# Kernel tuning notes

Hardware: AMD Instinct MI355X
Metric: run time of the kernel (lower is better)

Reference implementation:

```python
import jax, jax.numpy as jnp
import numpy as np

N = 50000          # nodes per side (variables == clauses here)
IN, HID, OUT = 64, 128, 128
H = 4              # attention heads (self and cross)
P = 2              # num_meta_paths
E = 640000         # edges per graph
NEG = 0.2          # leaky_relu negative slope


def _glorot(key, shape):
    fan = shape[-2] + shape[-1]
    return (jax.random.normal(key, shape) * jnp.sqrt(2.0 / fan)).astype(jnp.float32)


def _ln(x, g, b):
    mu = x.mean(-1, keepdims=True)
    v = ((x - mu) ** 2).mean(-1, keepdims=True)
    return (x - mu) / jnp.sqrt(v + 1e-5) * g + b


def _segment_softmax(s, seg, num):
    # s: [E, H]; softmax over edges sharing the same seg id
    smax = jax.ops.segment_max(s, seg, num_segments=num)
    e = jnp.exp(s - smax[seg])
    den = jax.ops.segment_sum(e, seg, num_segments=num)
    return e / (den[seg] + 1e-16)


def _agg(alpha, feats, src, dst, num):
    # out[d, h, c] = sum_{e: dst[e]=d} alpha[e,h] * feats[src[e], c]
    gathered = feats[src]  # [E, C]
    outs = [jax.ops.segment_sum(alpha[:, h:h + 1] * gathered, dst, num_segments=num)
            for h in range(alpha.shape[1])]
    return jnp.stack(outs, axis=1)  # [num, H, C]


def _hga_self(x, adj, W, att_l, att_r, bias):
    # homogeneous HGAConv with self loops, concat=False (mean over heads)
    n = x.shape[0]
    xl = x @ W.T                      # [N, C]
    al = xl @ att_l                   # [N, H]
    ar = xl @ att_r                   # [N, H]
    loops = jnp.arange(n)
    src = jnp.concatenate([adj[0], loops])
    dst = jnp.concatenate([adj[1], loops])
    score = al[dst] + ar[src]         # edge_score: a_l[adj[1]] + a_r[adj[0]]
    alpha = _segment_softmax(jax.nn.leaky_relu(score, NEG), dst, n)
    out = _agg(alpha, xl, src, dst, n).mean(axis=1)  # [N, C]
    return out + bias


def _hga_cross(xv, xc, adj, Wl, Wr, att_l, att_r, bias):
    # bipartite HGAConv: adj[1] indexes var nodes, adj[0] indexes cls nodes
    n, m = xv.shape[0], xc.shape[0]
    xl = xv @ Wl.T
    xr = xc @ Wr.T
    al = xl @ att_l
    ar = xr @ att_r
    ar_ = xl @ att_r
    al_ = xr @ att_l
    c_idx, v_idx = adj[0], adj[1]
    score = al[v_idx] + ar[c_idx]        # -> normalized per var node
    score_ = ar_[v_idx] + al_[c_idx]     # transposed direction -> per cls node
    alpha = _segment_softmax(jax.nn.leaky_relu(score, NEG), v_idx, n)
    alpha_ = _segment_softmax(jax.nn.leaky_relu(score_, NEG), c_idx, m)
    out_var = _agg(alpha, xr, c_idx, v_idx, n).mean(axis=1) + bias   # [n, OUT]
    out_cls = _agg(alpha_, xl, v_idx, c_idx, m).mean(axis=1) + bias  # [m, OUT]
    return out_var, out_cls


def setup_inputs() -> dict:
    key = jax.random.key(0)
    ks = jax.random.split(key, 32)
    d = {}
    d['x_var'] = jax.random.normal(ks[0], (N, IN), dtype=jnp.float32)
    d['x_cls'] = jax.random.normal(ks[1], (N, IN), dtype=jnp.float32)
    d['mp_var'] = jax.random.randint(ks[2], (P, 2, E), 0, N)
    d['mp_cls'] = jax.random.randint(ks[3], (P, 2, E), 0, N)
    d['adj_pos'] = jax.random.randint(ks[4], (2, E), 0, N)
    d['adj_neg'] = jax.random.randint(ks[5], (2, E), 0, N)
    d['W_var_emb'] = _glorot(ks[6], (HID, IN))
    d['W_cls_emb'] = _glorot(ks[7], (HID, IN))
    d['ln_var_g'] = jnp.ones(HID); d['ln_var_b'] = jnp.zeros(HID)
    d['ln_cls_g'] = jnp.ones(HID); d['ln_cls_b'] = jnp.zeros(HID)
    d['var_pw'] = jnp.ones(P); d['cls_pw'] = jnp.ones(P)
    d['sv_W'] = _glorot(ks[8], (P, HID, HID))
    d['sv_al'] = _glorot(ks[9], (P, HID, H))
    d['sv_ar'] = _glorot(ks[10], (P, HID, H))
    d['sv_b'] = jnp.zeros((P, HID))
    d['sc_W'] = _glorot(ks[11], (P, HID, HID))
    d['sc_al'] = _glorot(ks[12], (P, HID, H))
    d['sc_ar'] = _glorot(ks[13], (P, HID, H))
    d['sc_b'] = jnp.zeros((P, HID))
    d['cp_Wl'] = _glorot(ks[14], (OUT, HID))
    d['cp_Wr'] = _glorot(ks[15], (OUT, HID))
    d['cp_al'] = _glorot(ks[16], (OUT, H))
    d['cp_ar'] = _glorot(ks[17], (OUT, H))
    d['cp_b'] = jnp.zeros(OUT)
    d['cn_Wl'] = _glorot(ks[18], (OUT, HID))
    d['cn_Wr'] = _glorot(ks[19], (OUT, HID))
    d['cn_al'] = _glorot(ks[20], (OUT, H))
    d['cn_ar'] = _glorot(ks[21], (OUT, H))
    d['cn_b'] = jnp.zeros(OUT)
    return d


def reference(x_var, x_cls, mp_var, mp_cls, adj_pos, adj_neg,
              W_var_emb, W_cls_emb, ln_var_g, ln_var_b, ln_cls_g, ln_cls_b,
              var_pw, cls_pw, sv_W, sv_al, sv_ar, sv_b, sc_W, sc_al, sc_ar, sc_b,
              cp_Wl, cp_Wr, cp_al, cp_ar, cp_b, cn_Wl, cn_Wr, cn_al, cn_ar, cn_b):
    xv = x_var @ W_var_emb.T          # [N, HID]
    xc = x_cls @ W_cls_emb.T
    # pre-norm residual self-attention, weighted sum over meta paths
    hv = _ln(xv, ln_var_g, ln_var_b)
    hc = _ln(xc, ln_cls_g, ln_cls_b)
    av = sum(var_pw[p] * _hga_self(hv, mp_var[p], sv_W[p], sv_al[p], sv_ar[p], sv_b[p]) for p in range(P))
    ac = sum(cls_pw[p] * _hga_self(hc, mp_cls[p], sc_W[p], sc_al[p], sc_ar[p], sc_b[p]) for p in range(P))
    xv = xv + av
    xc = xc + ac
    # bipartite cross attention over positive / negative literal edges
    vpos, cpos = _hga_cross(xv, xc, adj_pos, cp_Wl, cp_Wr, cp_al, cp_ar, cp_b)
    vneg, cneg = _hga_cross(xv, xc, adj_neg, cn_Wl, cn_Wr, cn_al, cn_ar, cn_b)
    return jnp.stack([vpos + vneg, cpos + cneg])  # [2, N, OUT]
```

## Files before the change

kernel.cpp:

```cpp
#include <hip/hip_runtime.h>
#include <hip/hip_bf16.h>

#define NN 50000
#define EE 640000
#define NEG 0.2f
#define CAP 128

#define BSH 9
#define NBKT 98
#define FCAP 7168
#define CHUNKA 8192
#define PA_B 79

struct Ptr8 { const int* p[8]; };
struct MArgs { const float* w[8]; const float* al[8]; const float* ar[8]; };

struct SegArg {
    const int* starts;
    const int* counts;
    const unsigned short* srt;
    const float* adst;
    const float* asrc;
    const unsigned short* feats;
    const float* pw;
    int pwi;
    int hasLoop;
};

typedef __attribute__((ext_vector_type(8))) short short8;
typedef __attribute__((ext_vector_type(8))) unsigned short ushort8;
typedef __attribute__((ext_vector_type(4))) float floatx4;

__device__ __forceinline__ unsigned short f2bf(float x) {
    unsigned b = __float_as_uint(x);
    b = b + 0x7fffu + ((b >> 16) & 1u);
    return (unsigned short)(b >> 16);
}

__global__ void transpose_emb(const float* __restrict__ wev, const float* __restrict__ wec,
                              float* __restrict__ out)
{
    int i = blockIdx.x * 256 + threadIdx.x;
    if (i < 8192) { out[i] = wev[(i & 127) * 64 + (i >> 7)]; return; }
    if (i < 16384) { int j = i - 8192; out[i] = wec[(j & 127) * 64 + (j >> 7)]; }
}

__global__ void make_M(MArgs a, float* __restrict__ Mbuf)
{
    int b = blockIdx.x;
    const float* W  = a.w[b];
    const float* AL = a.al[b];
    const float* AR = a.ar[b];
    for (int e = threadIdx.x; e < 1024; e += 256) {
        int k = e >> 3, h = e & 7;
        const float* att = (h < 4) ? AL : AR;
        int hh = h & 3;
        float s = 0.f;
        for (int c = 0; c < 128; c++) s += W[c * 128 + k] * att[c * 4 + hh];
        Mbuf[b * 1024 + e] = s;
    }
}

__global__ void embed_ln(const float* __restrict__ x, const float* __restrict__ Wt,
                         const float* __restrict__ g, const float* __restrict__ b,
                         const float* __restrict__ pw, const float* __restrict__ sb,
                         float* __restrict__ F, float* __restrict__ C)
{
    __shared__ float lx[8][64];
    __shared__ float red[2][8][2];
    int c = threadIdx.x;
    int n0 = blockIdx.x * 8;
    for (int t = c; t < 8 * 64; t += 128) {
        lx[t >> 6][t & 63] = x[(size_t)(n0 + (t >> 6)) * 64 + (t & 63)];
    }
    __syncthreads();
    float acc[8];
#pragma unroll
    for (int m = 0; m < 8; m++) acc[m] = 0.f;
    for (int k = 0; k < 64; k++) {
        float w = Wt[k * 128 + c];
#pragma unroll
        for (int m = 0; m < 8; m++) acc[m] += lx[m][k] * w;
    }
    int lane = c & 63, wv = c >> 6;
#pragma unroll
    for (int m = 0; m < 8; m++) {
        float s1 = acc[m], s2 = acc[m] * acc[m];
        for (int off = 32; off; off >>= 1) { s1 += __shfl_xor(s1, off); s2 += __shfl_xor(s2, off); }
        if (lane == 0) { red[wv][m][0] = s1; red[wv][m][1] = s2; }
    }
    __syncthreads();
    float biassum = pw[0] * sb[c] + pw[1] * sb[128 + c];
    float gg = g[c], bb = b[c];
#pragma unroll
    for (int m = 0; m < 8; m++) {
        float s1 = red[0][m][0] + red[1][m][0];
        float s2 = red[0][m][1] + red[1][m][1];
        float mu  = s1 * (1.f / 128.f);
        float var = s2 * (1.f / 128.f) - mu * mu;
        float inv = rsqrtf(var + 1e-5f);
        float v = acc[m];
        size_t idx = (size_t)(n0 + m) * 128 + c;
        F[idx] = v + biassum;
        C[idx] = (v - mu) * inv * gg + bb;
    }
}

__device__ __forceinline__ void stage_W(const float* __restrict__ W,
                                        unsigned short* __restrict__ WL, int t)
{
    for (int i = t; i < 2048; i += 256) {
        int n = i >> 4, c16 = i & 15;
        const float* src = W + n * 128 + c16 * 8;
        short8 v;
#pragma unroll
        for (int j = 0; j < 8; j++) v[j] = (short)f2bf(src[j]);
        *(short8*)&WL[(n * 16 + (c16 ^ (n & 15))) * 8] = v;
    }
}

__global__ __launch_bounds__(256) void mfma_proj2(
    const float* __restrict__ in,
    const float* __restrict__ W0, const float* __restrict__ W1,
    const float* __restrict__ M0, const float* __restrict__ M1,
    unsigned short* __restrict__ ob0, unsigned short* __restrict__ ob1,
    float4* __restrict__ dl0, float4* __restrict__ dr0,
    float4* __restrict__ dl1, float4* __restrict__ dr1)
{
    __shared__ unsigned short WL[16384];
    __shared__ float ML[2048];

    int t = threadIdx.x;
    stage_W(W0, WL, t);
    for (int i = t; i < 1024; i += 256) { ML[i] = M0[i]; ML[1024 + i] = M1[i]; }
    __syncthreads();

    int w = t >> 6, lane = t & 63;
    int ln = lane & 15, quad = lane >> 4;
    int rbase = blockIdx.x * 64 + w * 16;
    int row = rbase + ln;
    int arow = (row < NN) ? row : (NN - 1);

    short8 afrag[4];
    float p[16];
#pragma unroll
    for (int h = 0; h < 16; h++) p[h] = 0.f;
#pragma unroll
    for (int kc = 0; kc < 4; kc++) {
        int k0 = kc * 32 + quad * 8;
        const float* ap = in + (size_t)arow * 128 + k0;
        float av[8];
#pragma unroll
        for (int j = 0; j < 8; j++) av[j] = ap[j];
#pragma unroll
        for (int j = 0; j < 8; j++) {
            afrag[kc][j] = (short)f2bf(av[j]);
            const float* m0 = &ML[(k0 + j) * 8];
            const float* m1 = &ML[1024 + (k0 + j) * 8];
#pragma unroll
            for (int h = 0; h < 8; h++) { p[h] += av[j] * m0[h]; p[8 + h] += av[j] * m1[h]; }
        }
    }
#pragma unroll
    for (int h = 0; h < 16; h++) {
        p[h] += __shfl_xor(p[h], 16);
        p[h] += __shfl_xor(p[h], 32);
    }
    if (quad == 0 && row < NN) {
        dl0[row] = make_float4(p[0], p[1], p[2], p[3]);
        dr0[row] = make_float4(p[4], p[5], p[6], p[7]);
        dl1[row] = make_float4(p[8], p[9], p[10], p[11]);
        dr1[row] = make_float4(p[12], p[13], p[14], p[15]);
    }

#pragma unroll
    for (int ct = 0; ct < 8; ct++) {
        floatx4 acc = {0.f, 0.f, 0.f, 0.f};
#pragma unroll
        for (int kc = 0; kc < 4; kc++) {
            int c16 = kc * 4 + quad;
            int n = ct * 16 + ln;
            short8 bfr = *(const short8*)&WL[(n * 16 + (c16 ^ ln)) * 8];
            acc = __builtin_amdgcn_mfma_f32_16x16x32_bf16(afrag[kc], bfr, acc, 0, 0, 0);
        }
#pragma unroll
        for (int r = 0; r < 4; r++) {
            int rr = rbase + quad * 4 + r;
            if (rr < NN) ob0[(size_t)rr * 128 + ct * 16 + ln] = f2bf(acc[r]);
        }
    }
    __syncthreads();
    stage_W(W1, WL, t);
    __syncthreads();
#pragma unroll
    for (int ct = 0; ct < 8; ct++) {
        floatx4 acc = {0.f, 0.f, 0.f, 0.f};
#pragma unroll
        for (int kc = 0; kc < 4; kc++) {
            int c16 = kc * 4 + quad;
            int n = ct * 16 + ln;
            short8 bfr = *(const short8*)&WL[(n * 16 + (c16 ^ ln)) * 8];
            acc = __builtin_amdgcn_mfma_f32_16x16x32_bf16(afrag[kc], bfr, acc, 0, 0, 0);
        }
#pragma unroll
        for (int r = 0; r < 4; r++) {
            int rr = rbase + quad * 4 + r;
            if (rr < NN) ob1[(size_t)rr * 128 + ct * 16 + ln] = f2bf(acc[r]);
        }
    }
}

__global__ void zero_bcnt(int* __restrict__ p)
{
    int i = blockIdx.x * 256 + threadIdx.x;
    if (i < 8 * NBKT) p[i] = 0;
}

__global__ void bucket_count(Ptr8 dst, int* __restrict__ bcnt)
{
    __shared__ int h[NBKT];
    int l = blockIdx.x / PA_B, cb = blockIdx.x % PA_B;
    const int* dp = dst.p[l];
    for (int i = threadIdx.x; i < NBKT; i += 256) h[i] = 0;
    __syncthreads();
    int e0 = cb * CHUNKA;
    for (int i = threadIdx.x; i < CHUNKA; i += 256) {
        int e = e0 + i;
        if (e < EE) atomicAdd(&h[dp[e] >> BSH], 1);
    }
    __syncthreads();
    for (int i = threadIdx.x; i < NBKT; i += 256)
        if (h[i]) atomicAdd(&bcnt[l * NBKT + i], h[i]);
}

__global__ void bucket_scan(const int* __restrict__ bcnt, int* __restrict__ bstart,
                            int* __restrict__ bcur)
{
    __shared__ int sh[NBKT];
    int l = blockIdx.x;
    for (int i = threadIdx.x; i < NBKT; i += 256) sh[i] = bcnt[l * NBKT + i];
    __syncthreads();
    if (threadIdx.x == 0) {
        int acc = 0;
        for (int i = 0; i < NBKT; i++) { int t = sh[i]; sh[i] = acc; acc += t; }
    }
    __syncthreads();
    for (int i = threadIdx.x; i < NBKT; i += 256) {
        bstart[l * (NBKT + 1) + i] = sh[i];
        bcur[l * NBKT + i] = sh[i];
    }
    if (threadIdx.x == 0) bstart[l * (NBKT + 1) + NBKT] = EE;
}

__global__ void bucket_place(Ptr8 src, Ptr8 dst, int* __restrict__ bcur,
                             unsigned* __restrict__ recs)
{
    __shared__ int h[NBKT];
    __shared__ int base[NBKT];
    int l = blockIdx.x / PA_B, cb = blockIdx.x % PA_B;
    const int* sp = src.p[l];
    const int* dp = dst.p[l];
    for (int i = threadIdx.x; i < NBKT; i += 256) h[i] = 0;
    __syncthreads();
    int e0 = cb * CHUNKA;
    for (int i = threadIdx.x; i < CHUNKA; i += 256) {
        int e = e0 + i;
        if (e < EE) atomicAdd(&h[dp[e] >> BSH], 1);
    }
    __syncthreads();
    for (int i = threadIdx.x; i < NBKT; i += 256) {
        int c = h[i];
        base[i] = c ? atomicAdd(&bcur[l * NBKT + i], c) : 0;
        h[i] = 0;
    }
    __syncthreads();
    unsigned* rl = recs + (size_t)l * EE;
    for (int i = threadIdx.x; i < CHUNKA; i += 256) {
        int e = e0 + i;
        if (e >= EE) continue;
        int d = dp[e];
        int b = d >> BSH;
        int pos = base[b] + atomicAdd(&h[b], 1);
        rl[pos] = ((unsigned)sp[e] << 16) | (unsigned)d;
    }
}

__global__ __launch_bounds__(256) void bucket_final(
    const unsigned* __restrict__ recs, const int* __restrict__ bstart,
    int* __restrict__ starts8, int* __restrict__ counts8,
    unsigned short* __restrict__ sortedU)
{
    __shared__ unsigned R[FCAP];
    __shared__ int cnt[512];
    __shared__ int cur[512];
    __shared__ int psum[256];
    int l = blockIdx.x / NBKT, b = blockIdx.x % NBKT;
    int d0 = b << BSH;
    int nd = min(512, NN - d0);
    int ebase = bstart[l * (NBKT + 1) + b];
    int ecnt  = bstart[l * (NBKT + 1) + b + 1] - ebase;
    const unsigned* rp = recs + (size_t)l * EE + ebase;
    int t = threadIdx.x;
    bool inLds = (ecnt <= FCAP);

    for (int i = t; i < 512; i += 256) cnt[i] = 0;
    __syncthreads();
    for (int i = t; i < ecnt; i += 256) {
        unsigned r = rp[i];
        if (inLds) R[i] = r;
        atomicAdd(&cnt[(r & 0xffffu) - d0], 1);
    }
    __syncthreads();
    int s0 = cnt[2 * t] + cnt[2 * t + 1];
    psum[t] = s0;
    __syncthreads();
    for (int off = 1; off < 256; off <<= 1) {
        int x = (t >= off) ? psum[t - off] : 0;
        __syncthreads();
        psum[t] += x;
        __syncthreads();
    }
    int excl = psum[t] - s0;
    cur[2 * t] = excl;
    cur[2 * t + 1] = excl + cnt[2 * t];
    __syncthreads();
    for (int i = t; i < nd; i += 256) {
        starts8[l * NN + d0 + i] = ebase + cur[i];
        counts8[l * NN + d0 + i] = cnt[i];
    }
    __syncthreads();
    unsigned short* so = sortedU + (size_t)l * EE + ebase;
    for (int i = t; i < ecnt; i += 256) {
        unsigned r = inLds ? R[i] : rp[i];
        int dloc = (int)(r & 0xffffu) - d0;
        int pos = atomicAdd(&cur[dloc], 1);
        so[pos] = (unsigned short)(r >> 16);
    }
}

__global__ __launch_bounds__(256) void agg_fused(
    SegArg A, SegArg B,
    const float* __restrict__ bias0, const float* __restrict__ bias1,
    float* __restrict__ acc, int mode)
{
    __shared__ float4 exSh[4][CAP];
    __shared__ int    sSh[4][CAP + 8];
    __shared__ float  wSh[4][CAP + 8];
    __shared__ float  cmb[4][128];

    int t = threadIdx.x;
    int slot = t >> 6;
    int w = slot & 1;
    int dh = slot >> 1;
    int lane = t & 63;
    int d = blockIdx.x * 2 + dh;

    const SegArg S = w ? B : A;

    int base = S.starts[d];
    int k = S.counts[d];
    int kTot = k + S.hasLoop;

    float4 ad = *(const float4*)(S.adst + (size_t)d * 4);
    float p0 = 0.f, p1 = 0.f, p2 = 0.f, p3 = 0.f;
    for (int i = lane; i < kTot; i += 64) {
        int s = (i < k) ? (int)S.srt[base + i] : d;
        float4 as = *(const float4*)(S.asrc + (size_t)s * 4);
        float v0 = ad.x + as.x, v1 = ad.y + as.y, v2 = ad.z + as.z, v3 = ad.w + as.w;
        v0 = v0 > 0.f ? v0 : NEG * v0;
        v1 = v1 > 0.f ? v1 : NEG * v1;
        v2 = v2 > 0.f ? v2 : NEG * v2;
        v3 = v3 > 0.f ? v3 : NEG * v3;
        float e0 = __expf(v0), e1 = __expf(v1), e2 = __expf(v2), e3 = __expf(v3);
        if (i < CAP) { exSh[slot][i] = make_float4(e0, e1, e2, e3); sSh[slot][i] = s; }
        p0 += e0; p1 += e1; p2 += e2; p3 += e3;
    }
#pragma unroll
    for (int off = 32; off; off >>= 1) {
        p0 += __shfl_xor(p0, off); p1 += __shfl_xor(p1, off);
        p2 += __shfl_xor(p2, off); p3 += __shfl_xor(p3, off);
    }
    float scale = 0.25f * (S.pw ? S.pw[S.pwi] : 1.0f);
    float i0 = scale / (p0 + 1e-16f);
    float i1 = scale / (p1 + 1e-16f);
    float i2 = scale / (p2 + 1e-16f);
    float i3 = scale / (p3 + 1e-16f);

    int kW = kTot < CAP ? kTot : CAP;
    for (int i = lane; i < kW; i += 64) {
        float4 ex = exSh[slot][i];
        wSh[slot][i] = ex.x * i0 + ex.y * i1 + ex.z * i2 + ex.w * i3;
    }
    if (kTot <= CAP) {
        int nPad = (kTot + 7) & ~7;
        for (int i = kTot + lane; i < nPad; i += 64) { wSh[slot][i] = 0.f; sSh[slot][i] = 0; }
    }
    __syncthreads();

    if (kTot <= CAP) {
        int g = lane >> 4, c8 = lane & 15;
        float a[8];
#pragma unroll
        for (int i = 0; i < 8; i++) a[i] = 0.f;
        int nIter = (kTot + 7) >> 3;
        for (int it = 0; it < nIter; ++it) {
            int j0 = it * 8 + g;
            int j1 = j0 + 4;
            float w0 = wSh[slot][j0], w1 = wSh[slot][j1];
            int s0 = sSh[slot][j0], s1 = sSh[slot][j1];
            ushort8 v0 = *(const ushort8*)(S.feats + (size_t)s0 * 128 + c8 * 8);
            ushort8 v1 = *(const ushort8*)(S.feats + (size_t)s1 * 128 + c8 * 8);
#pragma unroll
            for (int i = 0; i < 8; i++) {
                a[i] += w0 * __uint_as_float((unsigned)(unsigned short)v0[i] << 16);
                a[i] += w1 * __uint_as_float((unsigned)(unsigned short)v1[i] << 16);
            }
        }
#pragma unroll
        for (int i = 0; i < 8; i++) {
            a[i] += __shfl_xor(a[i], 16);
            a[i] += __shfl_xor(a[i], 32);
        }
        if (lane < 16) {
#pragma unroll
            for (int i = 0; i < 8; i++) cmb[slot][lane * 8 + i] = a[i];
        }
    } else {
        float a0 = 0.f, a1 = 0.f;
        for (int j = 0; j < kTot; ++j) {
            float wgt; int s;
            if (j < CAP) { wgt = wSh[slot][j]; s = sSh[slot][j]; }
            else {
                s = (j < k) ? (int)S.srt[base + j] : d;
                float4 as = *(const float4*)(S.asrc + (size_t)s * 4);
                float v0 = ad.x + as.x, v1 = ad.y + as.y, v2 = ad.z + as.z, v3 = ad.w + as.w;
                v0 = v0 > 0.f ? v0 : NEG * v0;
                v1 = v1 > 0.f ? v1 : NEG * v1;
                v2 = v2 > 0.f ? v2 : NEG * v2;
                v3 = v3 > 0.f ? v3 : NEG * v3;
                wgt = __expf(v0) * i0 + __expf(v1) * i1 + __expf(v2) * i2 + __expf(v3) * i3;
            }
            unsigned v = *(const unsigned*)(S.feats + (size_t)s * 128 + 2 * lane);
            a0 += wgt * __uint_as_float(v << 16);
            a1 += wgt * __uint_as_float(v & 0xffff0000u);
        }
        cmb[slot][2 * lane] = a0;
        cmb[slot][2 * lane + 1] = a1;
    }
    __syncthreads();

    {
        int dh2 = t >> 7;
        int c = t & 127;
        int dd = blockIdx.x * 2 + dh2;
        float sum = cmb[dh2 * 2][c] + cmb[dh2 * 2 + 1][c];
        size_t idx = (size_t)dd * 128 + c;
        if (mode) acc[idx] = bias0[c] + bias1[c] + sum;
        else      acc[idx] += sum;
    }
}

extern "C" void kernel_launch(void* const* d_in, const int* in_sizes, int n_in,
                              void* d_out, int out_size, void* d_ws, size_t ws_size,
                              hipStream_t stream)
{
    const float* x_var   = (const float*)d_in[0];
    const float* x_cls   = (const float*)d_in[1];
    const int*   mp_var  = (const int*)d_in[2];
    const int*   mp_cls  = (const int*)d_in[3];
    const int*   adj_pos = (const int*)d_in[4];
    const int*   adj_neg = (const int*)d_in[5];
    const float* W_var_emb = (const float*)d_in[6];
    const float* W_cls_emb = (const float*)d_in[7];
    const float* ln_var_g = (const float*)d_in[8];
    const float* ln_var_b = (const float*)d_in[9];
    const float* ln_cls_g = (const float*)d_in[10];
    const float* ln_cls_b = (const float*)d_in[11];
    const float* var_pw = (const float*)d_in[12];
    const float* cls_pw = (const float*)d_in[13];
    const float* sv_W  = (const float*)d_in[14];
    const float* sv_al = (const float*)d_in[15];
    const float* sv_ar = (const float*)d_in[16];
    const float* sv_b  = (const float*)d_in[17];
    const float* sc_W  = (const float*)d_in[18];
    const float* sc_al = (const float*)d_in[19];
    const float* sc_ar = (const float*)d_in[20];
    const float* sc_b  = (const float*)d_in[21];
    const float* cp_Wl = (const float*)d_in[22];
    const float* cp_Wr = (const float*)d_in[23];
    const float* cp_al = (const float*)d_in[24];
    const float* cp_ar = (const float*)d_in[25];
    const float* cp_b  = (const float*)d_in[26];
    const float* cn_Wl = (const float*)d_in[27];
    const float* cn_Wr = (const float*)d_in[28];
    const float* cn_al = (const float*)d_in[29];
    const float* cn_ar = (const float*)d_in[30];
    const float* cn_b  = (const float*)d_in[31];

    float* out0 = (float*)d_out;
    float* out1 = out0 + (size_t)NN * 128;

    float* ws = (float*)d_ws;
    size_t off = 0;
    auto alloc = [&](size_t n) { float* p = ws + off; off += n; return p; };
    float* Wt   = alloc(16384);
    float* Mbuf = alloc(8 * 1024);
    float* F   = alloc((size_t)NN * 128);
    float* G   = alloc((size_t)NN * 128);
    float* C   = alloc((size_t)NN * 128);
    float* D   = alloc((size_t)NN * 128);
    unsigned short* B1 = (unsigned short*)alloc((size_t)NN * 64);
    unsigned short* B2 = (unsigned short*)alloc((size_t)NN * 64);
    float* dl   = alloc(NN * 4);
    float* dr   = alloc(NN * 4);
    float* dl2  = alloc(NN * 4);
    float* dr2  = alloc(NN * 4);
    float* dl3  = alloc(NN * 4);
    float* dr3  = alloc(NN * 4);
    float* dl4  = alloc(NN * 4);
    float* dr4  = alloc(NN * 4);
    int* counts8 = (int*)alloc(8 * NN);
    int* starts8 = (int*)alloc(8 * NN);
    int* bcnt    = (int*)alloc(8 * NBKT);
    int* bstart  = (int*)alloc(8 * (NBKT + 1));
    int* bcur    = (int*)alloc(8 * NBKT);
    unsigned* recs = (unsigned*)alloc((size_t)8 * EE);
    unsigned short* sortedU = (unsigned short*)alloc((size_t)4 * EE);

    unsigned short* Pc = (unsigned short*)C;
    unsigned short* Pd = (unsigned short*)C + (size_t)NN * 128;

    const float* WtEv = Wt;
    const float* WtEc = Wt + 8192;

    Ptr8 srcP, dstP;
    srcP.p[0] = mp_var;            dstP.p[0] = mp_var + EE;
    srcP.p[1] = mp_var + 2 * EE;   dstP.p[1] = mp_var + 3 * EE;
    srcP.p[2] = mp_cls;            dstP.p[2] = mp_cls + EE;
    srcP.p[3] = mp_cls + 2 * EE;   dstP.p[3] = mp_cls + 3 * EE;
    srcP.p[4] = adj_pos;           dstP.p[4] = adj_pos + EE;
    srcP.p[5] = adj_pos + EE;      dstP.p[5] = adj_pos;
    srcP.p[6] = adj_neg;           dstP.p[6] = adj_neg + EE;
    srcP.p[7] = adj_neg + EE;      dstP.p[7] = adj_neg;

    MArgs ma;
    ma.w[0] = sv_W;           ma.al[0] = sv_al;        ma.ar[0] = sv_ar;
    ma.w[1] = sv_W + 16384;   ma.al[1] = sv_al + 512;  ma.ar[1] = sv_ar + 512;
    ma.w[2] = sc_W;           ma.al[2] = sc_al;        ma.ar[2] = sc_ar;
    ma.w[3] = sc_W + 16384;   ma.al[3] = sc_al + 512;  ma.ar[3] = sc_ar + 512;
    ma.w[4] = cp_Wl;          ma.al[4] = cp_al;        ma.ar[4] = cp_ar;
    ma.w[5] = cp_Wr;          ma.al[5] = cp_al;        ma.ar[5] = cp_ar;
    ma.w[6] = cn_Wl;          ma.al[6] = cn_al;        ma.ar[6] = cn_ar;
    ma.w[7] = cn_Wr;          ma.al[7] = cn_al;        ma.ar[7] = cn_ar;

    zero_bcnt<<<(8 * NBKT + 255) / 256, 256, 0, stream>>>(bcnt);
    bucket_count<<<8 * PA_B, 256, 0, stream>>>(dstP, bcnt);
    bucket_scan<<<8, 256, 0, stream>>>(bcnt, bstart, bcur);
    bucket_place<<<8 * PA_B, 256, 0, stream>>>(srcP, dstP, bcur, recs);
    bucket_final<<<8 * NBKT, 256, 0, stream>>>(recs, bstart, starts8, counts8, sortedU);

    transpose_emb<<<64, 256, 0, stream>>>(W_var_emb, W_cls_emb, Wt);
    make_M<<<8, 256, 0, stream>>>(ma, Mbuf);
    embed_ln<<<NN / 8, 128, 0, stream>>>(x_var, WtEv, ln_var_g, ln_var_b, var_pw, sv_b, F, C);
    embed_ln<<<NN / 8, 128, 0, stream>>>(x_cls, WtEc, ln_cls_g, ln_cls_b, cls_pw, sc_b, G, D);

    const int PB = (NN + 63) / 64;

    for (int side = 0; side < 2; ++side) {
        const float* h    = side ? D : C;
        float*       accp = side ? G : F;
        const float* pw   = side ? cls_pw : var_pw;
        int s0 = side * 2, s1 = side * 2 + 1;
        mfma_proj2<<<PB, 256, 0, stream>>>(h, ma.w[s0], ma.w[s1],
                                           Mbuf + s0 * 1024, Mbuf + s1 * 1024,
                                           B1, B2,
                                           (float4*)dl, (float4*)dr,
                                           (float4*)dl2, (float4*)dr2);
        SegArg SA, SB;
        SA.starts = starts8 + s0 * NN; SA.counts = counts8 + s0 * NN;
        SA.srt = sortedU + (size_t)s0 * EE;
        SA.adst = dl;  SA.asrc = dr;  SA.feats = B1; SA.pw = pw; SA.pwi = 0; SA.hasLoop = 1;
        SB.starts = starts8 + s1 * NN; SB.counts = counts8 + s1 * NN;
        SB.srt = sortedU + (size_t)s1 * EE;
        SB.adst = dl2; SB.asrc = dr2; SB.feats = B2; SB.pw = pw; SB.pwi = 1; SB.hasLoop = 1;
        agg_fused<<<NN / 2, 256, 0, stream>>>(SA, SB, cp_b, cn_b, accp, 0);
    }

    mfma_proj2<<<PB, 256, 0, stream>>>(F, ma.w[4], ma.w[6],
                                       Mbuf + 4 * 1024, Mbuf + 6 * 1024,
                                       B1, Pc,
                                       (float4*)dl, (float4*)dr,
                                       (float4*)dl3, (float4*)dr3);
    mfma_proj2<<<PB, 256, 0, stream>>>(G, ma.w[5], ma.w[7],
                                       Mbuf + 5 * 1024, Mbuf + 7 * 1024,
                                       B2, Pd,
                                       (float4*)dl2, (float4*)dr2,
                                       (float4*)dl4, (float4*)dr4);

    {
        SegArg SA, SB;
        SA.starts = starts8 + 4 * NN; SA.counts = counts8 + 4 * NN;
        SA.srt = sortedU + (size_t)4 * EE;
        SA.adst = dl;  SA.asrc = dr2; SA.feats = B2; SA.pw = nullptr; SA.pwi = 0; SA.hasLoop = 0;
        SB.starts = starts8 + 6 * NN; SB.counts = counts8 + 6 * NN;
        SB.srt = sortedU + (size_t)6 * EE;
        SB.adst = dl3; SB.asrc = dr4; SB.feats = Pd; SB.pw = nullptr; SB.pwi = 0; SB.hasLoop = 0;
        agg_fused<<<NN / 2, 256, 0, stream>>>(SA, SB, cp_b, cn_b, out0, 1);
    }
    {
        SegArg SA, SB;
        SA.starts = starts8 + 5 * NN; SA.counts = counts8 + 5 * NN;
        SA.srt = sortedU + (size_t)5 * EE;
        SA.adst = dl2; SA.asrc = dr;  SA.feats = B1; SA.pw = nullptr; SA.pwi = 0; SA.hasLoop = 0;
        SB.starts = starts8 + 7 * NN; SB.counts = counts8 + 7 * NN;
        SB.srt = sortedU + (size_t)7 * EE;
        SB.adst = dl4; SB.asrc = dr3; SB.feats = Pc; SB.pw = nullptr; SB.pwi = 0; SB.hasLoop = 0;
        agg_fused<<<NN / 2, 256, 0, stream>>>(SA, SB, cp_b, cn_b, out1, 1);
    }
}
```

Before: 754.4 us.

## Remap agg_fused to 16-lane groups per segment, eight nodes per block

Rewrites the aggregation kernel so each destination-segment pair is handled by a 16-lane group instead of a full 64-lane wavefront, giving eight nodes per block. The block-level syncs and the LDS combine stage go away: the two segments are reduced with a shuffle and written directly with float4 stores. Exponentials are recomputed in a second pass instead of being cached in shared memory, and source ids are stored as ushort. With an average degree around 13, this is meant to cut idle lanes and raise occupancy. The trade-offs are a serial per-edge loop within each group, duplicated exp work, and a smaller LDS cap (64) that sends high-degree nodes down the slow recompute path.

```diff
diff --git a/kernel.cpp b/kernel.cpp
--- a/kernel.cpp
+++ b/kernel.cpp
@@ -4,7 +4,7 @@
 #define NN 50000
 #define EE 640000
 #define NEG 0.2f
-#define CAP 128
+#define CAP 64
 
 #define BSH 9
 #define NBKT 98
@@ -35,6 +35,15 @@
     unsigned b = __float_as_uint(x);
     b = b + 0x7fffu + ((b >> 16) & 1u);
     return (unsigned short)(b >> 16);
+}
+
+__device__ __forceinline__ float4 leakyexp4(float4 ad, float4 as) {
+    float v0 = ad.x + as.x, v1 = ad.y + as.y, v2 = ad.z + as.z, v3 = ad.w + as.w;
+    v0 = v0 > 0.f ? v0 : NEG * v0;
+    v1 = v1 > 0.f ? v1 : NEG * v1;
+    v2 = v2 > 0.f ? v2 : NEG * v2;
+    v3 = v3 > 0.f ? v3 : NEG * v3;
+    return make_float4(__expf(v0), __expf(v1), __expf(v2), __expf(v3));
 }
 
 __global__ void transpose_emb(const float* __restrict__ wev, const float* __restrict__ wec,
@@ -338,125 +347,107 @@
     }
 }
 
-__global__ __launch_bounds__(256) void agg_fused(
+__global__ __launch_bounds__(256, 8) void agg_fused(
     SegArg A, SegArg B,
     const float* __restrict__ bias0, const float* __restrict__ bias1,
     float* __restrict__ acc, int mode)
 {
-    __shared__ float4 exSh[4][CAP];
-    __shared__ int    sSh[4][CAP + 8];
-    __shared__ float  wSh[4][CAP + 8];
-    __shared__ float  cmb[4][128];
+    __shared__ float          wSh[16][CAP];
+    __shared__ unsigned short sSh[16][CAP];
 
     int t = threadIdx.x;
-    int slot = t >> 6;
-    int w = slot & 1;
-    int dh = slot >> 1;
-    int lane = t & 63;
-    int d = blockIdx.x * 2 + dh;
-
-    const SegArg S = w ? B : A;
-
-    int base = S.starts[d];
-    int k = S.counts[d];
-    int kTot = k + S.hasLoop;
-
-    float4 ad = *(const float4*)(S.adst + (size_t)d * 4);
+    int gid = t >> 4;
+    int sub = t & 15;
+    int seg = gid & 1;
+    int d   = blockIdx.x * 8 + (gid >> 1);
+
+    const int* starts = seg ? B.starts : A.starts;
+    const int* counts = seg ? B.counts : A.counts;
+    const unsigned short* srt = seg ? B.srt : A.srt;
+    const float* adst = seg ? B.adst : A.adst;
+    const float* asrc = seg ? B.asrc : A.asrc;
+    const unsigned short* feats = seg ? B.feats : A.feats;
+    const float* pw = seg ? B.pw : A.pw;
+    int pwi = seg ? B.pwi : A.pwi;
+    int hasLoop = seg ? B.hasLoop : A.hasLoop;
+
+    int base = starts[d];
+    int k = counts[d];
+    int kTot = k + hasLoop;
+
+    float4 ad = *(const float4*)(adst + (size_t)d * 4);
+
     float p0 = 0.f, p1 = 0.f, p2 = 0.f, p3 = 0.f;
-    for (int i = lane; i < kTot; i += 64) {
-        int s = (i < k) ? (int)S.srt[base + i] : d;
-        float4 as = *(const float4*)(S.asrc + (size_t)s * 4);
-        float v0 = ad.x + as.x, v1 = ad.y + as.y, v2 = ad.z + as.z, v3 = ad.w + as.w;
-        v0 = v0 > 0.f ? v0 : NEG * v0;
-        v1 = v1 > 0.f ? v1 : NEG * v1;
-        v2 = v2 > 0.f ? v2 : NEG * v2;
-        v3 = v3 > 0.f ? v3 : NEG * v3;
-        float e0 = __expf(v0), e1 = __expf(v1), e2 = __expf(v2), e3 = __expf(v3);
-        if (i < CAP) { exSh[slot][i] = make_float4(e0, e1, e2, e3); sSh[slot][i] = s; }
-        p0 += e0; p1 += e1; p2 += e2; p3 += e3;
-    }
-#pragma unroll
-    for (int off = 32; off; off >>= 1) {
+    for (int i = sub; i < kTot; i += 16) {
+        int s = (i < k) ? (int)srt[base + i] : d;
+        if (i < CAP) sSh[gid][i] = (unsigned short)s;
+        float4 as = *(const float4*)(asrc + (size_t)s * 4);
+        float4 e = leakyexp4(ad, as);
+        p0 += e.x; p1 += e.y; p2 += e.z; p3 += e.w;
+    }
+#pragma unroll
+    for (int off = 1; off <= 8; off <<= 1) {
         p0 += __shfl_xor(p0, off); p1 += __shfl_xor(p1, off);
         p2 += __shfl_xor(p2, off); p3 += __shfl_xor(p3, off);
     }
-    float scale = 0.25f * (S.pw ? S.pw[S.pwi] : 1.0f);
+    float scale = 0.25f * (pw ? pw[pwi] : 1.0f);
     float i0 = scale / (p0 + 1e-16f);
     float i1 = scale / (p1 + 1e-16f);
     float i2 = scale / (p2 + 1e-16f);
     float i3 = scale / (p3 + 1e-16f);
 
     int kW = kTot < CAP ? kTot : CAP;
-    for (int i = lane; i < kW; i += 64) {
-        float4 ex = exSh[slot][i];
-        wSh[slot][i] = ex.x * i0 + ex.y * i1 + ex.z * i2 + ex.w * i3;
-    }
-    if (kTot <= CAP) {
-        int nPad = (kTot + 7) & ~7;
-        for (int i = kTot + lane; i < nPad; i += 64) { wSh[slot][i] = 0.f; sSh[slot][i] = 0; }
-    }
-    __syncthreads();
-
-    if (kTot <= CAP) {
-        int g = lane >> 4, c8 = lane & 15;
-        float a[8];
-#pragma unroll
-        for (int i = 0; i < 8; i++) a[i] = 0.f;
-        int nIter = (kTot + 7) >> 3;
-        for (int it = 0; it < nIter; ++it) {
-            int j0 = it * 8 + g;
-            int j1 = j0 + 4;
-            float w0 = wSh[slot][j0], w1 = wSh[slot][j1];
-            int s0 = sSh[slot][j0], s1 = sSh[slot][j1];
-            ushort8 v0 = *(const ushort8*)(S.feats + (size_t)s0 * 128 + c8 * 8);
-            ushort8 v1 = *(const ushort8*)(S.feats + (size_t)s1 * 128 + c8 * 8);
-#pragma unroll
-            for (int i = 0; i < 8; i++) {
-                a[i] += w0 * __uint_as_float((unsigned)(unsigned short)v0[i] << 16);
-                a[i] += w1 * __uint_as_float((unsigned)(unsigned short)v1[i] << 16);
-            }
+    for (int i = sub; i < kW; i += 16) {
+        int s = (int)sSh[gid][i];
+        float4 as = *(const float4*)(asrc + (size_t)s * 4);
+        float4 e = leakyexp4(ad, as);
+        wSh[gid][i] = e.x * i0 + e.y * i1 + e.z * i2 + e.w * i3;
+    }
+
+    float a[8];
+#pragma unroll
+    for (int i = 0; i < 8; i++) a[i] = 0.f;
+    const unsigned short* fbase = feats + sub * 8;
+    for (int j = 0; j < kW; ++j) {
+        float wgt = wSh[gid][j];
+        int s = (int)sSh[gid][j];
+        ushort8 v = *(const ushort8*)(fbase + (size_t)s * 128);
+#pragma unroll
+        for (int i = 0; i < 8; i++)
+            a[i] += wgt * __uint_as_float((unsigned)(unsigned short)v[i] << 16);
+    }
+    for (int j = CAP; j < kTot; ++j) {
+        int s = (j < k) ? (int)srt[base + j] : d;
+        float4 as = *(const float4*)(asrc + (size_t)s * 4);
+        float4 e = leakyexp4(ad, as);
+        float wgt = e.x * i0 + e.y * i1 + e.z * i2 + e.w * i3;
+        ushort8 v = *(const ushort8*)(fbase + (size_t)s * 128);
+#pragma unroll
+        for (int i = 0; i < 8; i++)
+            a[i] += wgt * __uint_as_float((unsigned)(unsigned short)v[i] << 16);
+    }
+
+#pragma unroll
+    for (int i = 0; i < 8; i++) a[i] += __shfl_xor(a[i], 16);
+
+    if (seg == 0) {
+        size_t idx = (size_t)d * 128 + sub * 8;
+        float4* ap = (float4*)(acc + idx);
+        float4 lo = make_float4(a[0], a[1], a[2], a[3]);
+        float4 hi = make_float4(a[4], a[5], a[6], a[7]);
+        if (mode) {
+            const float4* b0 = (const float4*)(bias0 + sub * 8);
+            const float4* b1 = (const float4*)(bias1 + sub * 8);
+            float4 c0 = b0[0], c1 = b0[1], d0v = b1[0], d1v = b1[1];
+            ap[0] = make_float4(c0.x + d0v.x + lo.x, c0.y + d0v.y + lo.y,
+                                c0.z + d0v.z + lo.z, c0.w + d0v.w + lo.w);
+            ap[1] = make_float4(c1.x + d1v.x + hi.x, c1.y + d1v.y + hi.y,
+                                c1.z + d1v.z + hi.z, c1.w + d1v.w + hi.w);
+        } else {
+            float4 r0 = ap[0], r1 = ap[1];
+            ap[0] = make_float4(r0.x + lo.x, r0.y + lo.y, r0.z + lo.z, r0.w + lo.w);
+            ap[1] = make_float4(r1.x + hi.x, r1.y + hi.y, r1.z + hi.z, r1.w + hi.w);
         }
-#pragma unroll
-        for (int i = 0; i < 8; i++) {
-            a[i] += __shfl_xor(a[i], 16);
-            a[i] += __shfl_xor(a[i], 32);
-        }
-        if (lane < 16) {
-#pragma unroll
-            for (int i = 0; i < 8; i++) cmb[slot][lane * 8 + i] = a[i];
-        }
-    } else {
-        float a0 = 0.f, a1 = 0.f;
-        for (int j = 0; j < kTot; ++j) {
-            float wgt; int s;
-            if (j < CAP) { wgt = wSh[slot][j]; s = sSh[slot][j]; }
-            else {
-                s = (j < k) ? (int)S.srt[base + j] : d;
-                float4 as = *(const float4*)(S.asrc + (size_t)s * 4);
-                float v0 = ad.x + as.x, v1 = ad.y + as.y, v2 = ad.z + as.z, v3 = ad.w + as.w;
-                v0 = v0 > 0.f ? v0 : NEG * v0;
-                v1 = v1 > 0.f ? v1 : NEG * v1;
-                v2 = v2 > 0.f ? v2 : NEG * v2;
-                v3 = v3 > 0.f ? v3 : NEG * v3;
-                wgt = __expf(v0) * i0 + __expf(v1) * i1 + __expf(v2) * i2 + __expf(v3) * i3;
-            }
-            unsigned v = *(const unsigned*)(S.feats + (size_t)s * 128 + 2 * lane);
-            a0 += wgt * __uint_as_float(v << 16);
-            a1 += wgt * __uint_as_float(v & 0xffff0000u);
-        }
-        cmb[slot][2 * lane] = a0;
-        cmb[slot][2 * lane + 1] = a1;
-    }
-    __syncthreads();
-
-    {
-        int dh2 = t >> 7;
-        int c = t & 127;
-        int dd = blockIdx.x * 2 + dh2;
-        float sum = cmb[dh2 * 2][c] + cmb[dh2 * 2 + 1][c];
-        size_t idx = (size_t)dd * 128 + c;
-        if (mode) acc[idx] = bias0[c] + bias1[c] + sum;
-        else      acc[idx] += sum;
     }
 }
 
@@ -565,6 +556,7 @@
     embed_ln<<<NN / 8, 128, 0, stream>>>(x_cls, WtEc, ln_cls_g, ln_cls_b, cls_pw, sc_b, G, D);
 
     const int PB = (NN + 63) / 64;
+    const int AB = NN / 8;
 
     for (int side = 0; side < 2; ++side) {
         const float* h    = side ? D : C;
@@ -583,7 +575,7 @@
         SB.starts = starts8 + s1 * NN; SB.counts = counts8 + s1 * NN;
         SB.srt = sortedU + (size_t)s1 * EE;
         SB.adst = dl2; SB.asrc = dr2; SB.feats = B2; SB.pw = pw; SB.pwi = 1; SB.hasLoop = 1;
-        agg_fused<<<NN / 2, 256, 0, stream>>>(SA, SB, cp_b, cn_b, accp, 0);
+        agg_fused<<<AB, 256, 0, stream>>>(SA, SB, cp_b, cn_b, accp, 0);
     }
 
     mfma_proj2<<<PB, 256, 0, stream>>>(F, ma.w[4], ma.w[6],
@@ -605,7 +597,7 @@
         SB.starts = starts8 + 6 * NN; SB.counts = counts8 + 6 * NN;
         SB.srt = sortedU + (size_t)6 * EE;
         SB.adst = dl3; SB.asrc = dr4; SB.feats = Pd; SB.pw = nullptr; SB.pwi = 0; SB.hasLoop = 0;
-        agg_fused<<<NN / 2, 256, 0, stream>>>(SA, SB, cp_b, cn_b, out0, 1);
+        agg_fused<<<AB, 256, 0, stream>>>(SA, SB, cp_b, cn_b, out0, 1);
     }
     {
         SegArg SA, SB;
@@ -615,6 +607,6 @@
         SB.starts = starts8 + 7 * NN; SB.counts = counts8 + 7 * NN;
         SB.srt = sortedU + (size_t)7 * EE;
         SB.adst = dl4; SB.asrc = dr3; SB.feats = Pc; SB.pw = nullptr; SB.pwi = 0; SB.hasLoop = 0;
-        agg_fused<<<NN / 2, 256, 0, stream>>>(SA, SB, cp_b, cn_b, out1, 1);
-    }
-}
+        agg_fused<<<AB, 256, 0, stream>>>(SA, SB, cp_b, cn_b, out1, 1);
+    }
+}
```

Measured after the change: 729.3 us. -3.3%, faster.
